# Optimization experiments

Hardware: AMD Instinct MI355X
Metric: run time of the kernel (lower is better)

Reference implementation:

```python
import jax, jax.numpy as jnp
import numpy as np

N = 50000
E = 800000
IN = 128
H = 128
OUT = 64
L = 2
THETA = 1.0
SCALE = 2.0


def setup_inputs() -> dict:
    key = jax.random.key(0)
    ks = jax.random.split(key, 12)
    g = lambda k, s: (jax.random.normal(k, s, jnp.float32) * 0.05)
    return {
        "x": jax.random.normal(ks[0], (N, IN), jnp.float32),
        "edge_index": jax.random.randint(ks[1], (2, E), 0, N),
        "mlp_w1": g(ks[2], (IN, 512)), "mlp_b1": jnp.zeros((512,), jnp.float32),
        "mlp_w2": g(ks[3], (512, 64)), "mlp_b2": jnp.zeros((64,), jnp.float32),
        "mlp_w3": g(ks[4], (64, OUT)), "mlp_b3": jnp.zeros((OUT,), jnp.float32),
        "parsing": jnp.ones((L, OUT, OUT), jnp.float32) / SCALE,
        "lin0_w": g(ks[5], (IN, H)), "lin0_b": jnp.zeros((H,), jnp.float32),
        "lin1_w": g(ks[6], (H, OUT)), "lin1_b": jnp.zeros((OUT,), jnp.float32),
        "conv_w1": g(ks[7], (L, H, H)),
        "conv_w2": g(ks[8], (L, H, H)),
    }


def reference(x, edge_index, mlp_w1, mlp_b1, mlp_w2, mlp_b2, mlp_w3, mlp_b3,
              parsing, lin0_w, lin0_b, lin1_w, lin1_b, conv_w1, conv_w2):
    row, col = edge_index[0], edge_index[1]  # start, end

    # --- learn_soft_edge3 (algebraically exact reduction of outer-product + bmm + diag) ---
    h = jax.nn.relu(x @ mlp_w1 + mlp_b1)
    h = jax.nn.relu(h @ mlp_w2 + mlp_b2)
    logits = h @ mlp_w3 + mlp_b3                      # [N, OUT]
    P = jax.nn.relu(SCALE * parsing[0])               # [OUT, OUT]
    # diag(outer(start,end) @ P)[e,c] = start[e,c] * (end @ P)[e,c]
    ew = jnp.sum(logits[row] * (logits @ P)[col], axis=1)  # [E]
    mean = ew.mean()
    var = jnp.var(ew, ddof=1)                          # torch.var is unbiased
    ew = (ew - mean) * jnp.sqrt(jnp.float32(1e-4) / var) + 1.0

    # --- GCN2 stack ---
    x0 = jax.nn.relu(x @ lin0_w + lin0_b)              # [N, H]
    # gcn_norm with self loops (weight 1)
    loop = jnp.arange(N)
    r = jnp.concatenate([row, loop])
    c = jnp.concatenate([col, loop])
    w = jnp.concatenate([ew, jnp.ones((N,), ew.dtype)])
    deg = jax.ops.segment_sum(w, c, num_segments=N)
    dinv = jnp.where(deg > 0, jax.lax.rsqrt(jnp.where(deg > 0, deg, 1.0)), 0.0)
    norm = dinv[r] * w * dinv[c]                       # [E+N]

    hcur = x0
    alpha = 0.0
    for ln in range(L):
        agg = jax.ops.segment_sum(norm[:, None] * hcur[r], c, num_segments=N)  # [N, H]
        agg = agg * (1.0 - alpha)
        x0a = alpha * x0
        beta = float(np.log(THETA / (ln + 1) + 1.0))
        out = (1.0 - beta) * agg + beta * (agg @ conv_w1[ln]) \
            + (1.0 - beta) * x0a + beta * (x0a @ conv_w2[ln])
        hcur = jax.nn.relu(out)
    return hcur @ lin1_w + lin1_b                      # [N, OUT]
```

## Files before the change

### kernel.cpp

```cpp
#include <hip/hip_runtime.h>
#include <hip/hip_bf16.h>
#include <hip/hip_fp16.h>
#include <math.h>

#define NN 50000
#define NE 800000

typedef __attribute__((ext_vector_type(8))) short bf16x8;
typedef __attribute__((ext_vector_type(4))) float f32x4;

__device__ __forceinline__ short f2bf(float f){
  unsigned u = __float_as_uint(f);
  unsigned r = (u + 0x7fffu + ((u >> 16) & 1u)) >> 16;
  return (short)r;
}
__device__ __forceinline__ float bf2f(short s){
  return __uint_as_float(((unsigned)(unsigned short)s) << 16);
}

__device__ __forceinline__ unsigned f2fp8(float f){
  __half h = __float2half(f * 0.00390625f);
  unsigned hb = (unsigned)__half_as_ushort(h);
  unsigned s = hb >> 15;
  unsigned mag = hb & 0x7fffu;
  mag = mag + 0x3fu + ((mag >> 7) & 1u);
  unsigned m8 = mag >> 7;
  if (m8 > 0x7eu) m8 = 0x7eu;
  return (s << 7) | m8;
}
__device__ __forceinline__ void fp8x4_dec(unsigned u, float2& lo, float2& hi){
  unsigned l = ((u & 0x80u) << 8) | ((u & 0x7fu) << 7)
             | ((u & 0x8000u) << 16) | ((u & 0x7f00u) << 15);
  unsigned h = ((u & 0x800000u) >> 8) | ((u & 0x7f0000u) >> 9)
             | (u & 0x80000000u) | ((u & 0x7f000000u) >> 1);
  __half2 hl = *(__half2*)&l;
  __half2 hh = *(__half2*)&h;
  lo = __half22float2(hl);
  hi = __half22float2(hh);
}
__device__ __forceinline__ float fp8_dot4(unsigned a, unsigned b){
  float2 al, ah, bl, bh;
  fp8x4_dec(a, al, ah); fp8x4_dec(b, bl, bh);
  return al.x*bl.x + al.y*bl.y + ah.x*bh.x + ah.y*bh.y;
}

__global__ __launch_bounds__(256) void prep_k(const float* __restrict__ w1,
    const float* __restrict__ w2, const float* __restrict__ w3, const float* __restrict__ pars,
    const float* __restrict__ lin0w, const float* __restrict__ cw1, const float* __restrict__ lin1w,
    short* __restrict__ w1t, short* __restrict__ w2t, short* __restrict__ w3t, short* __restrict__ Pt,
    short* __restrict__ lin0wt, short* __restrict__ cw1t0, short* __restrict__ cw1t1,
    short* __restrict__ lin1wt, int* __restrict__ cnt, float* __restrict__ scal){
  int idx = blockIdx.x*256 + threadIdx.x;
  if (idx < NN) cnt[idx] = 0;
  if (idx < 16) scal[idx] = 0.0f;
  if (idx < 65536){
    int n = idx >> 7, k = idx & 127;
    w1t[idx] = f2bf(w1[k*512 + n]);
  } else if (idx < 98304){
    int i = idx - 65536; int n = i >> 9, k = i & 511;
    w2t[i] = f2bf(w2[k*64 + n]);
  } else if (idx < 102400){
    int i = idx - 98304; int n = i >> 6, k = i & 63;
    w3t[i] = f2bf(w3[k*64 + n]);
  } else if (idx < 106496){
    int i = idx - 102400; int n = i >> 6, k = i & 63;
    Pt[i] = f2bf(fmaxf(2.f*pars[k*64 + n], 0.f));
  } else if (idx < 122880){
    int i = idx - 106496; int n = i >> 7, k = i & 127;
    lin0wt[i] = f2bf(lin0w[k*128 + n]);
  } else if (idx < 139264){
    int i = idx - 122880; int n = i >> 7, k = i & 127;
    cw1t0[i] = f2bf(cw1[k*128 + n]);
  } else if (idx < 155648){
    int i = idx - 139264; int n = i >> 7, k = i & 127;
    cw1t1[i] = f2bf(cw1[16384 + k*128 + n]);
  } else if (idx < 163840){
    int i = idx - 155648; int n = i >> 7, k = i & 127;
    lin1wt[i] = f2bf(lin1w[k*64 + n]);
  }
}

__global__ __launch_bounds__(256) void mlp_mfma_k(
    const float* __restrict__ x,
    const short* __restrict__ w1t, const float* __restrict__ b1,
    const short* __restrict__ w2t, const float* __restrict__ b2,
    const short* __restrict__ w3t, const float* __restrict__ b3,
    const short* __restrict__ Pt,
    unsigned char* __restrict__ lg8, unsigned char* __restrict__ lgp8,
    short* __restrict__ xb, int M)
{
  __shared__ short xs [64][132];
  __shared__ short h1s[64][260];
  __shared__ short h2s[64][68];
  __shared__ short lgs[64][68];
  const int t = threadIdx.x;
  const int wave = t >> 6, lane = t & 63;
  const int quad = lane >> 4, l16 = lane & 15;
  const int m0 = blockIdx.x * 64;

  for (int task = t; task < 1024; task += 256){
    int row = task >> 4, c0 = (task & 15) * 8;
    float4 v0 = make_float4(0,0,0,0), v1 = v0;
    int gm = m0 + row;
    if (gm < M){
      v0 = *(const float4*)(x + (size_t)gm*128 + c0);
      v1 = *(const float4*)(x + (size_t)gm*128 + c0 + 4);
    }
    bf16x8 s;
    s[0]=f2bf(v0.x); s[1]=f2bf(v0.y); s[2]=f2bf(v0.z); s[3]=f2bf(v0.w);
    s[4]=f2bf(v1.x); s[5]=f2bf(v1.y); s[6]=f2bf(v1.z); s[7]=f2bf(v1.w);
    *(bf16x8*)&xs[row][c0] = s;
    if (gm < M) *(bf16x8*)(xb + (size_t)gm*128 + c0) = s;
  }
  __syncthreads();

  f32x4 acc2a[4], acc2b[4];
  #pragma unroll
  for (int mt=0;mt<4;mt++){ acc2a[mt] = (f32x4){0.f,0.f,0.f,0.f}; acc2b[mt] = acc2a[mt]; }
  const int n2 = wave*16 + l16;

  #pragma unroll
  for (int half = 0; half < 2; half++){
    {
      f32x4 acc[4][4];
      #pragma unroll
      for (int mt=0;mt<4;mt++)
        #pragma unroll
        for (int nt=0;nt<4;nt++) acc[mt][nt] = (f32x4){0.f,0.f,0.f,0.f};
      #pragma unroll
      for (int k0 = 0; k0 < 128; k0 += 32){
        bf16x8 a0 = *(const bf16x8*)&xs[l16     ][k0 + quad*8];
        bf16x8 a1 = *(const bf16x8*)&xs[16 + l16][k0 + quad*8];
        bf16x8 a2 = *(const bf16x8*)&xs[32 + l16][k0 + quad*8];
        bf16x8 a3 = *(const bf16x8*)&xs[48 + l16][k0 + quad*8];
        #pragma unroll
        for (int nt = 0; nt < 4; nt++){
          int n = half*256 + wave*64 + nt*16 + l16;
          bf16x8 b = *(const bf16x8*)(w1t + (size_t)n*128 + k0 + quad*8);
          acc[0][nt] = __builtin_amdgcn_mfma_f32_16x16x32_bf16(a0, b, acc[0][nt], 0,0,0);
          acc[1][nt] = __builtin_amdgcn_mfma_f32_16x16x32_bf16(a1, b, acc[1][nt], 0,0,0);
          acc[2][nt] = __builtin_amdgcn_mfma_f32_16x16x32_bf16(a2, b, acc[2][nt], 0,0,0);
          acc[3][nt] = __builtin_amdgcn_mfma_f32_16x16x32_bf16(a3, b, acc[3][nt], 0,0,0);
        }
      }
      #pragma unroll
      for (int nt = 0; nt < 4; nt++){
        int n  = half*256 + wave*64 + nt*16 + l16;
        int cl = wave*64 + nt*16 + l16;
        float bb = b1[n];
        #pragma unroll
        for (int mt = 0; mt < 4; mt++){
          #pragma unroll
          for (int r = 0; r < 4; r++){
            int row = mt*16 + quad*4 + r;
            h1s[row][cl] = f2bf(fmaxf(acc[mt][nt][r] + bb, 0.f));
          }
        }
      }
    }
    __syncthreads();

    #pragma unroll
    for (int k0 = 0; k0 < 128; k0 += 32){
      bf16x8 bA = *(const bf16x8*)(w2t + (size_t)n2*512 + half*256 + k0 + quad*8);
      bf16x8 bB = *(const bf16x8*)(w2t + (size_t)n2*512 + half*256 + 128 + k0 + quad*8);
      #pragma unroll
      for (int mt = 0; mt < 4; mt++){
        bf16x8 aA = *(const bf16x8*)&h1s[mt*16 + l16][k0 + quad*8];
        bf16x8 aB = *(const bf16x8*)&h1s[mt*16 + l16][128 + k0 + quad*8];
        acc2a[mt] = __builtin_amdgcn_mfma_f32_16x16x32_bf16(aA, bA, acc2a[mt], 0,0,0);
        acc2b[mt] = __builtin_amdgcn_mfma_f32_16x16x32_bf16(aB, bB, acc2b[mt], 0,0,0);
      }
    }
    if (half == 0) __syncthreads();
  }

  {
    float bb = b2[n2];
    #pragma unroll
    for (int mt = 0; mt < 4; mt++)
      #pragma unroll
      for (int r = 0; r < 4; r++)
        h2s[mt*16 + quad*4 + r][n2] = f2bf(fmaxf(acc2a[mt][r] + acc2b[mt][r] + bb, 0.f));
  }
  __syncthreads();

  {
    f32x4 acc[4];
    #pragma unroll
    for (int mt=0;mt<4;mt++) acc[mt] = (f32x4){0.f,0.f,0.f,0.f};
    #pragma unroll
    for (int k0 = 0; k0 < 64; k0 += 32){
      bf16x8 b = *(const bf16x8*)(w3t + (size_t)n2*64 + k0 + quad*8);
      #pragma unroll
      for (int mt = 0; mt < 4; mt++){
        bf16x8 a = *(const bf16x8*)&h2s[mt*16 + l16][k0 + quad*8];
        acc[mt] = __builtin_amdgcn_mfma_f32_16x16x32_bf16(a, b, acc[mt], 0,0,0);
      }
    }
    float bb = b3[n2];
    #pragma unroll
    for (int mt = 0; mt < 4; mt++)
      #pragma unroll
      for (int r = 0; r < 4; r++)
        lgs[mt*16 + quad*4 + r][n2] = f2bf(acc[mt][r] + bb);
  }
  __syncthreads();

  {
    f32x4 acc[4];
    #pragma unroll
    for (int mt=0;mt<4;mt++) acc[mt] = (f32x4){0.f,0.f,0.f,0.f};
    #pragma unroll
    for (int k0 = 0; k0 < 64; k0 += 32){
      bf16x8 b = *(const bf16x8*)(Pt + (size_t)n2*64 + k0 + quad*8);
      #pragma unroll
      for (int mt = 0; mt < 4; mt++){
        bf16x8 a = *(const bf16x8*)&lgs[mt*16 + l16][k0 + quad*8];
        acc[mt] = __builtin_amdgcn_mfma_f32_16x16x32_bf16(a, b, acc[mt], 0,0,0);
      }
    }
    #pragma unroll
    for (int mt = 0; mt < 4; mt++)
      #pragma unroll
      for (int r = 0; r < 4; r++)
        h2s[mt*16 + quad*4 + r][n2] = f2bf(acc[mt][r]);
  }
  __syncthreads();

  {
    int row = t >> 2, c0 = (t & 3) * 16;
    int gm = m0 + row;
    if (gm < M){
      const short* pl = &lgs[row][c0];
      const short* pp = &h2s[row][c0];
      unsigned a[4] = {0,0,0,0}, b[4] = {0,0,0,0};
      #pragma unroll
      for (int q2 = 0; q2 < 4; q2++){
        #pragma unroll
        for (int j = 0; j < 4; j++){
          a[q2] |= f2fp8(bf2f(pl[q2*4+j])) << (8*j);
          b[q2] |= f2fp8(bf2f(pp[q2*4+j])) << (8*j);
        }
      }
      uint4 av; av.x=a[0]; av.y=a[1]; av.z=a[2]; av.w=a[3];
      uint4 bv; bv.x=b[0]; bv.y=b[1]; bv.z=b[2]; bv.w=b[3];
      *(uint4*)(lg8  + (size_t)gm*64 + c0) = av;
      *(uint4*)(lgp8 + (size_t)gm*64 + c0) = bv;
    }
  }
}

template<int NT, bool RELU, bool RESID, bool BF16OUT, bool SCALEROW>
__global__ __launch_bounds__(256) void bgemm_k(
    const short* __restrict__ A, const short* __restrict__ Bt,
    const float* __restrict__ bias, const short* __restrict__ extra,
    const float* __restrict__ dinvp,
    float* __restrict__ C, short* __restrict__ Cb, int M, float beta)
{
  const int N = NT*64;
  __shared__ short As[32][136];
  const int t = threadIdx.x;
  const int wave = t >> 6, lane = t & 63;
  const int quad = lane >> 4, l16 = lane & 15;
  const int m0 = blockIdx.x * 32;

  for (int task = t; task < 512; task += 256){
    int row = task >> 4, c0 = (task & 15) * 8;
    bf16x8 v = {0,0,0,0,0,0,0,0};
    if (m0 + row < M) v = *(const bf16x8*)(A + (size_t)(m0+row)*128 + c0);
    *(bf16x8*)&As[row][c0] = v;
  }
  __syncthreads();

  f32x4 acc[2][NT];
  #pragma unroll
  for (int mt=0;mt<2;mt++)
    #pragma unroll
    for (int nt=0;nt<NT;nt++) acc[mt][nt] = (f32x4){0.f,0.f,0.f,0.f};

  #pragma unroll
  for (int k0 = 0; k0 < 128; k0 += 32){
    bf16x8 a0 = *(const bf16x8*)&As[l16     ][k0 + quad*8];
    bf16x8 a1 = *(const bf16x8*)&As[16 + l16][k0 + quad*8];
    #pragma unroll
    for (int nt = 0; nt < NT; nt++){
      int n = (wave*NT + nt)*16 + l16;
      bf16x8 b = *(const bf16x8*)(Bt + (size_t)n*128 + k0 + quad*8);
      acc[0][nt] = __builtin_amdgcn_mfma_f32_16x16x32_bf16(a0, b, acc[0][nt], 0,0,0);
      acc[1][nt] = __builtin_amdgcn_mfma_f32_16x16x32_bf16(a1, b, acc[1][nt], 0,0,0);
    }
  }

  #pragma unroll
  for (int nt = 0; nt < NT; nt++){
    int n = (wave*NT + nt)*16 + l16;
    float bb = (bias != nullptr) ? bias[n] : 0.f;
    #pragma unroll
    for (int mt = 0; mt < 2; mt++){
      #pragma unroll
      for (int r = 0; r < 4; r++){
        int gm = m0 + mt*16 + quad*4 + r;
        if (gm >= M) continue;
        float v = acc[mt][nt][r];
        if (RESID){
          float ex = bf2f(extra[(size_t)gm*N + n]);
          v = beta*v + (1.f - beta)*ex;
        }
        v += bb;
        if (RELU) v = fmaxf(v, 0.f);
        if (SCALEROW) v *= dinvp[gm];
        if (BF16OUT) Cb[(size_t)gm*N + n] = f2bf(v);
        else         C [(size_t)gm*N + n] = v;
      }
    }
  }
}

__global__ __launch_bounds__(256) void count_k(const int* __restrict__ col, int* __restrict__ cnt,
    int* __restrict__ rank, int E){
  int i = (blockIdx.x*256 + threadIdx.x)*4;
  if (i + 3 < E){
    int4 c = *(const int4*)(col + i);
    int r0 = atomicAdd(&cnt[c.x], 1);
    int r1 = atomicAdd(&cnt[c.y], 1);
    int r2 = atomicAdd(&cnt[c.z], 1);
    int r3 = atomicAdd(&cnt[c.w], 1);
    *(int4*)(rank + i) = make_int4(r0, r1, r2, r3);
  } else {
    for (; i < E; i++) rank[i] = atomicAdd(&cnt[col[i]], 1);
  }
}

__global__ __launch_bounds__(256) void scan_sums_k(const int* __restrict__ cnt, int* __restrict__ bsum, int n){
  __shared__ int s[256];
  const int t = threadIdx.x;
  int i = blockIdx.x*1024 + t*4;
  int4 v = make_int4(0,0,0,0);
  if (i + 3 < n) v = *(const int4*)(cnt + i);
  else {
    if (i   < n) v.x = cnt[i];
    if (i+1 < n) v.y = cnt[i+1];
    if (i+2 < n) v.z = cnt[i+2];
    if (i+3 < n) v.w = cnt[i+3];
  }
  s[t] = v.x + v.y + v.z + v.w;
  __syncthreads();
  for (int st = 128; st; st >>= 1){
    if (t < st) s[t] += s[t + st];
    __syncthreads();
  }
  if (t == 0) bsum[blockIdx.x] = s[0];
}

__global__ __launch_bounds__(256) void scan_final_k(const int* __restrict__ cnt, const int* __restrict__ bsum,
    int* __restrict__ off, int n, int total, int nb){
  __shared__ int s[256];
  __shared__ int basebs;
  const int t = threadIdx.x;
  if (t < 64){
    int v = (t < nb && t < (int)blockIdx.x) ? bsum[t] : 0;
    #pragma unroll
    for (int o = 1; o < 64; o <<= 1) v += __shfl_xor(v, o);
    if (t == 0) basebs = v;
  }
  int i = blockIdx.x*1024 + t*4;
  int4 v = make_int4(0,0,0,0);
  if (i + 3 < n) v = *(const int4*)(cnt + i);
  else {
    if (i   < n) v.x = cnt[i];
    if (i+1 < n) v.y = cnt[i+1];
    if (i+2 < n) v.z = cnt[i+2];
    if (i+3 < n) v.w = cnt[i+3];
  }
  int tsum = v.x + v.y + v.z + v.w;
  s[t] = tsum;
  __syncthreads();
  #pragma unroll
  for (int st = 1; st < 256; st <<= 1){
    int a = (t >= st) ? s[t - st] : 0;
    __syncthreads();
    s[t] += a;
    __syncthreads();
  }
  int base = s[t] - tsum + basebs;
  int o0 = base, o1 = o0 + v.x, o2 = o1 + v.y, o3 = o2 + v.z;
  if (i   < n) off[i]   = o0;
  if (i+1 < n) off[i+1] = o1;
  if (i+2 < n) off[i+2] = o2;
  if (i+3 < n) off[i+3] = o3;
  if (blockIdx.x == 0 && t == 0) off[n] = total;
}

__global__ __launch_bounds__(256) void scatter_k(const int* __restrict__ row, const int* __restrict__ col,
    const int* __restrict__ off, const int* __restrict__ rank,
    int2* __restrict__ csr_sd, int E){
  int i = (blockIdx.x*256 + threadIdx.x)*4;
  if (i + 3 < E){
    int4 r = *(const int4*)(row + i);
    int4 c = *(const int4*)(col + i);
    int4 k = *(const int4*)(rank + i);
    int o0 = off[c.x], o1 = off[c.y], o2 = off[c.z], o3 = off[c.w];
    int2 p0; p0.x = r.x; p0.y = c.x;
    int2 p1; p1.x = r.y; p1.y = c.y;
    int2 p2; p2.x = r.z; p2.y = c.z;
    int2 p3; p3.x = r.w; p3.y = c.w;
    csr_sd[o0 + k.x] = p0;
    csr_sd[o1 + k.y] = p1;
    csr_sd[o2 + k.z] = p2;
    csr_sd[o3 + k.w] = p3;
  } else {
    for (; i < E; i++){
      int2 p; p.x = row[i]; p.y = col[i];
      csr_sd[off[col[i]] + rank[i]] = p;
    }
  }
}

__global__ __launch_bounds__(256) void ew2_k(const unsigned char* __restrict__ lg8,
    const unsigned char* __restrict__ lgp8,
    const int2* __restrict__ sd,
    float* __restrict__ w, float* __restrict__ scal, int E){
  const int t = threadIdx.x;
  const int lane = t & 63, wid = t >> 6;
  const int g = lane >> 4, q = lane & 15;
  const int gid = (blockIdx.x*4 + wid)*4 + g;
  const int ngroups = gridDim.x*16;
  float s = 0.f, ss = 0.f;
  for (int base = gid*8; base < E; base += ngroups*8){
    int4 p01 = *(const int4*)(sd + base);
    int4 p23 = *(const int4*)(sd + base + 2);
    int4 p45 = *(const int4*)(sd + base + 4);
    int4 p67 = *(const int4*)(sd + base + 6);
    unsigned a0 = *(const unsigned*)(lg8  + (size_t)p01.x*64 + q*4);
    unsigned a1 = *(const unsigned*)(lg8  + (size_t)p01.z*64 + q*4);
    unsigned a2 = *(const unsigned*)(lg8  + (size_t)p23.x*64 + q*4);
    unsigned a3 = *(const unsigned*)(lg8  + (size_t)p23.z*64 + q*4);
    unsigned a4 = *(const unsigned*)(lg8  + (size_t)p45.x*64 + q*4);
    unsigned a5 = *(const unsigned*)(lg8  + (size_t)p45.z*64 + q*4);
    unsigned a6 = *(const unsigned*)(lg8  + (size_t)p67.x*64 + q*4);
    unsigned a7 = *(const unsigned*)(lg8  + (size_t)p67.z*64 + q*4);
    unsigned b0 = *(const unsigned*)(lgp8 + (size_t)p01.y*64 + q*4);
    unsigned b1 = *(const unsigned*)(lgp8 + (size_t)p01.w*64 + q*4);
    unsigned b2 = *(const unsigned*)(lgp8 + (size_t)p23.y*64 + q*4);
    unsigned b3 = *(const unsigned*)(lgp8 + (size_t)p23.w*64 + q*4);
    unsigned b4 = *(const unsigned*)(lgp8 + (size_t)p45.y*64 + q*4);
    unsigned b5 = *(const unsigned*)(lgp8 + (size_t)p45.w*64 + q*4);
    unsigned b6 = *(const unsigned*)(lgp8 + (size_t)p67.y*64 + q*4);
    unsigned b7 = *(const unsigned*)(lgp8 + (size_t)p67.w*64 + q*4);
    float v0 = fp8_dot4(a0, b0);
    float v1 = fp8_dot4(a1, b1);
    float v2 = fp8_dot4(a2, b2);
    float v3 = fp8_dot4(a3, b3);
    float v4 = fp8_dot4(a4, b4);
    float v5 = fp8_dot4(a5, b5);
    float v6 = fp8_dot4(a6, b6);
    float v7 = fp8_dot4(a7, b7);
    #pragma unroll
    for (int o = 1; o < 16; o <<= 1){
      v0 += __shfl_xor(v0, o); v1 += __shfl_xor(v1, o);
      v2 += __shfl_xor(v2, o); v3 += __shfl_xor(v3, o);
      v4 += __shfl_xor(v4, o); v5 += __shfl_xor(v5, o);
      v6 += __shfl_xor(v6, o); v7 += __shfl_xor(v7, o);
    }
    if (q == 0){
      float4 va = make_float4(v0*65536.f, v1*65536.f, v2*65536.f, v3*65536.f);
      float4 vb = make_float4(v4*65536.f, v5*65536.f, v6*65536.f, v7*65536.f);
      *(float4*)(w + base)     = va;
      *(float4*)(w + base + 4) = vb;
      s  += va.x + va.y + va.z + va.w + vb.x + vb.y + vb.z + vb.w;
      ss += va.x*va.x + va.y*va.y + va.z*va.z + va.w*va.w
          + vb.x*vb.x + vb.y*vb.y + vb.z*vb.z + vb.w*vb.w;
    }
  }
  #pragma unroll
  for (int o = 1; o < 64; o <<= 1){ s += __shfl_xor(s, o); ss += __shfl_xor(ss, o); }
  __shared__ float ls[4], lss[4];
  if (lane == 0){ ls[wid] = s; lss[wid] = ss; }
  __syncthreads();
  if (t == 0){
    atomicAdd(&scal[0], ls[0]+ls[1]+ls[2]+ls[3]);
    atomicAdd(&scal[1], lss[0]+lss[1]+lss[2]+lss[3]);
  }
}

__global__ __launch_bounds__(256) void degnorm_k(float* __restrict__ w, const int* __restrict__ off,
    const float* __restrict__ scal, float* __restrict__ dinv, int Nn, int E){
  int n = blockIdx.x*256 + threadIdx.x;
  if (n < Nn){
    double sum = (double)scal[0], sumsq = (double)scal[1];
    double mean_d = sum / (double)E;
    double var    = (sumsq - sum*sum/(double)E) / (double)(E-1);
    float mean = (float)mean_d;
    float k    = (float)sqrt(1e-4 / var);
    int s = off[n], e = off[n+1];
    float d = 1.0f;
    for (int j = s; j < e; j++){
      float v = (w[j] - mean) * k + 1.0f;
      w[j] = v;
      d += v;
    }
    dinv[n] = (d > 0.f) ? rsqrtf(d) : 0.f;
  }
}

__global__ __launch_bounds__(256) void agg_gather_k(const short* __restrict__ hb,
    const int* __restrict__ off, const int2* __restrict__ sd, const float* __restrict__ w,
    const float* __restrict__ dinv, short* __restrict__ aggb, int Nn){
  int n = blockIdx.x*4 + (threadIdx.x >> 6);
  int lane = threadIdx.x & 63;
  if (n >= Nn) return;
  float d = dinv[n];
  short2 hv = *(const short2*)(hb + (size_t)n*128 + lane*2);
  float acc0 = bf2f(hv.x), acc1 = bf2f(hv.y);
  int s = off[n], e = off[n+1];
  int j = s;
  for (; j + 7 < e; j += 8){
    int4 p0 = *(const int4*)(sd + j);
    int4 p1 = *(const int4*)(sd + j + 2);
    int4 p2 = *(const int4*)(sd + j + 4);
    int4 p3 = *(const int4*)(sd + j + 6);
    float4 w0 = *(const float4*)(w + j);
    float4 w1 = *(const float4*)(w + j + 4);
    short2 h0 = *(const short2*)(hb + (size_t)p0.x*128 + lane*2);
    short2 h1 = *(const short2*)(hb + (size_t)p0.z*128 + lane*2);
    short2 h2 = *(const short2*)(hb + (size_t)p1.x*128 + lane*2);
    short2 h3 = *(const short2*)(hb + (size_t)p1.z*128 + lane*2);
    short2 h4 = *(const short2*)(hb + (size_t)p2.x*128 + lane*2);
    short2 h5 = *(const short2*)(hb + (size_t)p2.z*128 + lane*2);
    short2 h6 = *(const short2*)(hb + (size_t)p3.x*128 + lane*2);
    short2 h7 = *(const short2*)(hb + (size_t)p3.z*128 + lane*2);
    acc0 += w0.x*bf2f(h0.x) + w0.y*bf2f(h1.x) + w0.z*bf2f(h2.x) + w0.w*bf2f(h3.x)
          + w1.x*bf2f(h4.x) + w1.y*bf2f(h5.x) + w1.z*bf2f(h6.x) + w1.w*bf2f(h7.x);
    acc1 += w0.x*bf2f(h0.y) + w0.y*bf2f(h1.y) + w0.z*bf2f(h2.y) + w0.w*bf2f(h3.y)
          + w1.x*bf2f(h4.y) + w1.y*bf2f(h5.y) + w1.z*bf2f(h6.y) + w1.w*bf2f(h7.y);
  }
  for (; j < e; j++){
    int2 p = sd[j];
    short2 h0 = *(const short2*)(hb + (size_t)p.x*128 + lane*2);
    float w0 = w[j];
    acc0 += w0*bf2f(h0.x); acc1 += w0*bf2f(h0.y);
  }
  acc0 *= d; acc1 *= d;
  short2 o; o.x = f2bf(acc0); o.y = f2bf(acc1);
  *(short2*)(aggb + (size_t)n*128 + lane*2) = o;
}

extern "C" void kernel_launch(void* const* d_in, const int* in_sizes, int n_in,
                              void* d_out, int out_size, void* d_ws, size_t ws_size,
                              hipStream_t stream){
  const float* x      = (const float*)d_in[0];
  const int*   ei     = (const int*)  d_in[1];
  const float* w1     = (const float*)d_in[2];
  const float* b1     = (const float*)d_in[3];
  const float* w2     = (const float*)d_in[4];
  const float* b2     = (const float*)d_in[5];
  const float* w3     = (const float*)d_in[6];
  const float* b3     = (const float*)d_in[7];
  const float* pars   = (const float*)d_in[8];
  const float* lin0w  = (const float*)d_in[9];
  const float* lin0b  = (const float*)d_in[10];
  const float* lin1w  = (const float*)d_in[11];
  const float* lin1b  = (const float*)d_in[12];
  const float* cw1    = (const float*)d_in[13];
  float* out          = (float*)d_out;

  float* ws = (float*)d_ws;
  int*   cnt     = (int*)(ws + 0);
  int*   off     = (int*)(ws + 50048);
  int2*  csr_sd  = (int2*)(ws + 150144);
  int*   bsum    = (int*)(ws + 1750400);
  short* lin0wt  = (short*)(ws + 1751000);
  short* cw1t0   = lin0wt + 16384;
  short* cw1t1   = cw1t0 + 16384;
  short* lin1wt  = cw1t1 + 16384;
  unsigned char* lg8  = (unsigned char*)(ws + 1800000);
  unsigned char* lgp8 = (unsigned char*)(ws + 2600000);
  float* csr_w2  = ws + 3400000;
  float* dinv    = ws + 5800000;
  float* scal    = ws + 5850048;
  short* bufAb   = (short*)(ws + 5900000);
  short* bufCb   = (short*)(ws + 9100000);
  short* aggb    = (short*)(ws + 12300000);
  short* bufBb   = (short*)(ws + 15500000);
  short* w1t     = (short*)(ws + 18700000);
  short* w2t     = w1t + 65536;
  short* w3t     = w2t + 32768;
  short* Pt      = w3t + 4096;
  short* xb      = (short*)(ws + 18800000);
  int*   rank    = (int*)(ws + 22000000);

  const int Mn = NN, E = NE;
  const int* erow = ei;
  const int* ecol = ei + E;
  const float beta0 = 0.69314718055994530942f;
  const float beta1 = 0.40546510810816438198f;
  const int nScanB = (Mn + 1023) / 1024;
  const int nGB = (Mn + 31) / 32;
  const int nE4 = (E/4 + 255) / 256;

  prep_k<<<(163840+255)/256, 256, 0, stream>>>(w1, w2, w3, pars, lin0w, cw1, lin1w,
                                               w1t, w2t, w3t, Pt, lin0wt, cw1t0, cw1t1, lin1wt,
                                               cnt, scal);
  count_k<<<nE4, 256, 0, stream>>>(ecol, cnt, rank, E);
  scan_sums_k<<<nScanB, 256, 0, stream>>>(cnt, bsum, Mn);
  scan_final_k<<<nScanB, 256, 0, stream>>>(cnt, bsum, off, Mn, E, nScanB);
  scatter_k<<<nE4, 256, 0, stream>>>(erow, ecol, off, rank, csr_sd, E);
  mlp_mfma_k<<<(Mn+63)/64, 256, 0, stream>>>(x, w1t, b1, w2t, b2, w3t, b3, Pt,
                                             lg8, lgp8, xb, Mn);
  ew2_k<<<1024, 256, 0, stream>>>(lg8, lgp8, csr_sd, csr_w2, scal, E);
  degnorm_k<<<(Mn+255)/256, 256, 0, stream>>>(csr_w2, off, scal, dinv, Mn, E);
  bgemm_k<2,true,false,true,true><<<nGB, 256, 0, stream>>>(xb, lin0wt, lin0b, nullptr, dinv, nullptr, bufAb, Mn, 0.f);
  agg_gather_k<<<(Mn+3)/4, 256, 0, stream>>>(bufAb, off, csr_sd, csr_w2, dinv, aggb, Mn);
  bgemm_k<2,true,true,true,true><<<nGB, 256, 0, stream>>>(aggb, cw1t0, nullptr, aggb, dinv, nullptr, bufCb, Mn, beta0);
  agg_gather_k<<<(Mn+3)/4, 256, 0, stream>>>(bufCb, off, csr_sd, csr_w2, dinv, aggb, Mn);
  bgemm_k<2,true,true,true,false><<<nGB, 256, 0, stream>>>(aggb, cw1t1, nullptr, aggb, nullptr, nullptr, bufBb, Mn, beta1);
  bgemm_k<1,false,false,false,false><<<nGB, 256, 0, stream>>>(bufBb, lin1wt, lin1b, nullptr, nullptr, out, nullptr, Mn, 0.f);
}
```

Baseline: 366.4 us.

## Fold parsing matrix into w3 and fuse final conv GEMM with output linear

Precomputes w3·relu(2P) and b3·relu(2P) in the prep kernel, so the MLP kernel produces logits and logits@P from one shared pass over h2 instead of two chained GEMMs with an extra barrier. The last GCN2 layer GEMM and the lin1 projection now run in a single kernel that keeps the intermediate tile in shared memory, removing one launch and a bf16 round trip through global memory. The bgemm shared-memory row padding also changes from 136 to 132. In exchange, prep does 64-term dot products per thread, and logits@P is no longer computed from bf16-rounded logits, which changes rounding slightly.

```diff
diff --git a/kernel.cpp b/kernel.cpp
--- a/kernel.cpp
+++ b/kernel.cpp
@@ -46,8 +46,10 @@
 
 __global__ __launch_bounds__(256) void prep_k(const float* __restrict__ w1,
     const float* __restrict__ w2, const float* __restrict__ w3, const float* __restrict__ pars,
-    const float* __restrict__ lin0w, const float* __restrict__ cw1, const float* __restrict__ lin1w,
-    short* __restrict__ w1t, short* __restrict__ w2t, short* __restrict__ w3t, short* __restrict__ Pt,
+    const float* __restrict__ b3, const float* __restrict__ lin0w, const float* __restrict__ cw1,
+    const float* __restrict__ lin1w,
+    short* __restrict__ w1t, short* __restrict__ w2t, short* __restrict__ w3t,
+    short* __restrict__ w3pt, float* __restrict__ b3P,
     short* __restrict__ lin0wt, short* __restrict__ cw1t0, short* __restrict__ cw1t1,
     short* __restrict__ lin1wt, int* __restrict__ cnt, float* __restrict__ scal){
   int idx = blockIdx.x*256 + threadIdx.x;
@@ -63,8 +65,11 @@
     int i = idx - 98304; int n = i >> 6, k = i & 63;
     w3t[i] = f2bf(w3[k*64 + n]);
   } else if (idx < 106496){
-    int i = idx - 102400; int n = i >> 6, k = i & 63;
-    Pt[i] = f2bf(fmaxf(2.f*pars[k*64 + n], 0.f));
+    int i = idx - 102400; int c = i >> 6, k = i & 63;
+    float s = 0.f;
+    for (int j = 0; j < 64; j++)
+      s += w3[k*64 + j] * fmaxf(2.f*pars[j*64 + c], 0.f);
+    w3pt[i] = f2bf(s);
   } else if (idx < 122880){
     int i = idx - 106496; int n = i >> 7, k = i & 127;
     lin0wt[i] = f2bf(lin0w[k*128 + n]);
@@ -77,6 +82,11 @@
   } else if (idx < 163840){
     int i = idx - 155648; int n = i >> 7, k = i & 127;
     lin1wt[i] = f2bf(lin1w[k*64 + n]);
+  } else if (idx < 163904){
+    int c = idx - 163840;
+    float s = 0.f;
+    for (int j = 0; j < 64; j++) s += b3[j] * fmaxf(2.f*pars[j*64 + c], 0.f);
+    b3P[c] = s;
   }
 }
 
@@ -85,7 +95,7 @@
     const short* __restrict__ w1t, const float* __restrict__ b1,
     const short* __restrict__ w2t, const float* __restrict__ b2,
     const short* __restrict__ w3t, const float* __restrict__ b3,
-    const short* __restrict__ Pt,
+    const short* __restrict__ w3pt, const float* __restrict__ b3P,
     unsigned char* __restrict__ lg8, unsigned char* __restrict__ lgp8,
     short* __restrict__ xb, int M)
 {
@@ -186,45 +196,29 @@
   __syncthreads();
 
   {
-    f32x4 acc[4];
-    #pragma unroll
-    for (int mt=0;mt<4;mt++) acc[mt] = (f32x4){0.f,0.f,0.f,0.f};
+    f32x4 accL[4], accP[4];
+    #pragma unroll
+    for (int mt=0;mt<4;mt++){ accL[mt] = (f32x4){0.f,0.f,0.f,0.f}; accP[mt] = accL[mt]; }
     #pragma unroll
     for (int k0 = 0; k0 < 64; k0 += 32){
-      bf16x8 b = *(const bf16x8*)(w3t + (size_t)n2*64 + k0 + quad*8);
+      bf16x8 bL = *(const bf16x8*)(w3t  + (size_t)n2*64 + k0 + quad*8);
+      bf16x8 bP = *(const bf16x8*)(w3pt + (size_t)n2*64 + k0 + quad*8);
       #pragma unroll
       for (int mt = 0; mt < 4; mt++){
         bf16x8 a = *(const bf16x8*)&h2s[mt*16 + l16][k0 + quad*8];
-        acc[mt] = __builtin_amdgcn_mfma_f32_16x16x32_bf16(a, b, acc[mt], 0,0,0);
-      }
-    }
-    float bb = b3[n2];
+        accL[mt] = __builtin_amdgcn_mfma_f32_16x16x32_bf16(a, bL, accL[mt], 0,0,0);
+        accP[mt] = __builtin_amdgcn_mfma_f32_16x16x32_bf16(a, bP, accP[mt], 0,0,0);
+      }
+    }
+    __syncthreads();
+    float bbL = b3[n2], bbP = b3P[n2];
     #pragma unroll
     for (int mt = 0; mt < 4; mt++)
       #pragma unroll
-      for (int r = 0; r < 4; r++)
-        lgs[mt*16 + quad*4 + r][n2] = f2bf(acc[mt][r] + bb);
-  }
-  __syncthreads();
-
-  {
-    f32x4 acc[4];
-    #pragma unroll
-    for (int mt=0;mt<4;mt++) acc[mt] = (f32x4){0.f,0.f,0.f,0.f};
-    #pragma unroll
-    for (int k0 = 0; k0 < 64; k0 += 32){
-      bf16x8 b = *(const bf16x8*)(Pt + (size_t)n2*64 + k0 + quad*8);
-      #pragma unroll
-      for (int mt = 0; mt < 4; mt++){
-        bf16x8 a = *(const bf16x8*)&lgs[mt*16 + l16][k0 + quad*8];
-        acc[mt] = __builtin_amdgcn_mfma_f32_16x16x32_bf16(a, b, acc[mt], 0,0,0);
-      }
-    }
-    #pragma unroll
-    for (int mt = 0; mt < 4; mt++)
-      #pragma unroll
-      for (int r = 0; r < 4; r++)
-        h2s[mt*16 + quad*4 + r][n2] = f2bf(acc[mt][r]);
+      for (int r = 0; r < 4; r++){
+        lgs[mt*16 + quad*4 + r][n2] = f2bf(accL[mt][r] + bbL);
+        h2s[mt*16 + quad*4 + r][n2] = f2bf(accP[mt][r] + bbP);
+      }
   }
   __syncthreads();
 
@@ -259,7 +253,7 @@
     float* __restrict__ C, short* __restrict__ Cb, int M, float beta)
 {
   const int N = NT*64;
-  __shared__ short As[32][136];
+  __shared__ short As[32][132];
   const int t = threadIdx.x;
   const int wave = t >> 6, lane = t & 63;
   const int quad = lane >> 4, l16 = lane & 15;
@@ -315,6 +309,87 @@
       }
     }
   }
+}
+
+__global__ __launch_bounds__(256) void bgemm_fuse_k(
+    const short* __restrict__ A, const short* __restrict__ Bt,
+    const short* __restrict__ extra,
+    const short* __restrict__ lin1wt, const float* __restrict__ lin1b,
+    float* __restrict__ out, int M, float beta)
+{
+  __shared__ short As[32][132];
+  const int t = threadIdx.x;
+  const int wave = t >> 6, lane = t & 63;
+  const int quad = lane >> 4, l16 = lane & 15;
+  const int m0 = blockIdx.x * 32;
+
+  for (int task = t; task < 512; task += 256){
+    int row = task >> 4, c0 = (task & 15) * 8;
+    bf16x8 v = {0,0,0,0,0,0,0,0};
+    if (m0 + row < M) v = *(const bf16x8*)(A + (size_t)(m0+row)*128 + c0);
+    *(bf16x8*)&As[row][c0] = v;
+  }
+  __syncthreads();
+
+  f32x4 acc[2][2];
+  #pragma unroll
+  for (int mt=0;mt<2;mt++)
+    #pragma unroll
+    for (int nt=0;nt<2;nt++) acc[mt][nt] = (f32x4){0.f,0.f,0.f,0.f};
+
+  #pragma unroll
+  for (int k0 = 0; k0 < 128; k0 += 32){
+    bf16x8 a0 = *(const bf16x8*)&As[l16     ][k0 + quad*8];
+    bf16x8 a1 = *(const bf16x8*)&As[16 + l16][k0 + quad*8];
+    #pragma unroll
+    for (int nt = 0; nt < 2; nt++){
+      int n = (wave*2 + nt)*16 + l16;
+      bf16x8 b = *(const bf16x8*)(Bt + (size_t)n*128 + k0 + quad*8);
+      acc[0][nt] = __builtin_amdgcn_mfma_f32_16x16x32_bf16(a0, b, acc[0][nt], 0,0,0);
+      acc[1][nt] = __builtin_amdgcn_mfma_f32_16x16x32_bf16(a1, b, acc[1][nt], 0,0,0);
+    }
+  }
+  __syncthreads();
+
+  #pragma unroll
+  for (int nt = 0; nt < 2; nt++){
+    int n = (wave*2 + nt)*16 + l16;
+    #pragma unroll
+    for (int mt = 0; mt < 2; mt++){
+      #pragma unroll
+      for (int r = 0; r < 4; r++){
+        int row = mt*16 + quad*4 + r;
+        int gm = m0 + row;
+        float v = 0.f;
+        if (gm < M){
+          float ex = bf2f(extra[(size_t)gm*128 + n]);
+          v = fmaxf(beta*acc[mt][nt][r] + (1.f - beta)*ex, 0.f);
+        }
+        As[row][n] = f2bf(v);
+      }
+    }
+  }
+  __syncthreads();
+
+  f32x4 acc2[2];
+  acc2[0] = (f32x4){0.f,0.f,0.f,0.f}; acc2[1] = acc2[0];
+  const int n2 = wave*16 + l16;
+  #pragma unroll
+  for (int k0 = 0; k0 < 128; k0 += 32){
+    bf16x8 b  = *(const bf16x8*)(lin1wt + (size_t)n2*128 + k0 + quad*8);
+    bf16x8 a0 = *(const bf16x8*)&As[l16     ][k0 + quad*8];
+    bf16x8 a1 = *(const bf16x8*)&As[16 + l16][k0 + quad*8];
+    acc2[0] = __builtin_amdgcn_mfma_f32_16x16x32_bf16(a0, b, acc2[0], 0,0,0);
+    acc2[1] = __builtin_amdgcn_mfma_f32_16x16x32_bf16(a1, b, acc2[1], 0,0,0);
+  }
+  float bb = lin1b[n2];
+  #pragma unroll
+  for (int mt = 0; mt < 2; mt++)
+    #pragma unroll
+    for (int r = 0; r < 4; r++){
+      int gm = m0 + mt*16 + quad*4 + r;
+      if (gm < M) out[(size_t)gm*64 + n2] = acc2[mt][r] + bb;
+    }
 }
 
 __global__ __launch_bounds__(256) void count_k(const int* __restrict__ col, int* __restrict__ cnt,
@@ -579,14 +654,14 @@
   float* csr_w2  = ws + 3400000;
   float* dinv    = ws + 5800000;
   float* scal    = ws + 5850048;
+  float* b3P     = ws + 5850064;
   short* bufAb   = (short*)(ws + 5900000);
   short* bufCb   = (short*)(ws + 9100000);
   short* aggb    = (short*)(ws + 12300000);
-  short* bufBb   = (short*)(ws + 15500000);
   short* w1t     = (short*)(ws + 18700000);
   short* w2t     = w1t + 65536;
   short* w3t     = w2t + 32768;
-  short* Pt      = w3t + 4096;
+  short* w3pt    = w3t + 4096;
   short* xb      = (short*)(ws + 18800000);
   int*   rank    = (int*)(ws + 22000000);
 
@@ -599,14 +674,14 @@
   const int nGB = (Mn + 31) / 32;
   const int nE4 = (E/4 + 255) / 256;
 
-  prep_k<<<(163840+255)/256, 256, 0, stream>>>(w1, w2, w3, pars, lin0w, cw1, lin1w,
-                                               w1t, w2t, w3t, Pt, lin0wt, cw1t0, cw1t1, lin1wt,
-                                               cnt, scal);
+  prep_k<<<(163904+255)/256, 256, 0, stream>>>(w1, w2, w3, pars, b3, lin0w, cw1, lin1w,
+                                               w1t, w2t, w3t, w3pt, b3P,
+                                               lin0wt, cw1t0, cw1t1, lin1wt, cnt, scal);
   count_k<<<nE4, 256, 0, stream>>>(ecol, cnt, rank, E);
   scan_sums_k<<<nScanB, 256, 0, stream>>>(cnt, bsum, Mn);
   scan_final_k<<<nScanB, 256, 0, stream>>>(cnt, bsum, off, Mn, E, nScanB);
   scatter_k<<<nE4, 256, 0, stream>>>(erow, ecol, off, rank, csr_sd, E);
-  mlp_mfma_k<<<(Mn+63)/64, 256, 0, stream>>>(x, w1t, b1, w2t, b2, w3t, b3, Pt,
+  mlp_mfma_k<<<(Mn+63)/64, 256, 0, stream>>>(x, w1t, b1, w2t, b2, w3t, b3, w3pt, b3P,
                                              lg8, lgp8, xb, Mn);
   ew2_k<<<1024, 256, 0, stream>>>(lg8, lgp8, csr_sd, csr_w2, scal, E);
   degnorm_k<<<(Mn+255)/256, 256, 0, stream>>>(csr_w2, off, scal, dinv, Mn, E);
@@ -614,6 +689,5 @@
   agg_gather_k<<<(Mn+3)/4, 256, 0, stream>>>(bufAb, off, csr_sd, csr_w2, dinv, aggb, Mn);
   bgemm_k<2,true,true,true,true><<<nGB, 256, 0, stream>>>(aggb, cw1t0, nullptr, aggb, dinv, nullptr, bufCb, Mn, beta0);
   agg_gather_k<<<(Mn+3)/4, 256, 0, stream>>>(bufCb, off, csr_sd, csr_w2, dinv, aggb, Mn);
-  bgemm_k<2,true,true,true,false><<<nGB, 256, 0, stream>>>(aggb, cw1t1, nullptr, aggb, nullptr, nullptr, bufBb, Mn, beta1);
-  bgemm_k<1,false,false,false,false><<<nGB, 256, 0, stream>>>(bufBb, lin1wt, lin1b, nullptr, nullptr, out, nullptr, Mn, 0.f);
-}
+  bgemm_fuse_k<<<nGB, 256, 0, stream>>>(aggb, cw1t1, aggb, lin1wt, lin1b, out, Mn, beta1);
+}
```

New measurement: 360.8 us (median of 3 runs). No clear change (-1.5%).
